# Performance work log

Measured on AMD Instinct MI355X. Metric: run time of the kernel, lower is better.

Reference implementation:

```python
import jax, jax.numpy as jnp
import numpy as np
import math

B, S, H, NH = 2, 2048, 1024, 16
DK = H // NH


def setup_inputs() -> dict:
    key = jax.random.key(0)
    ks = jax.random.split(key, 12)
    s = 1.0 / math.sqrt(H)
    return {
        "query": jax.random.normal(ks[0], (B, S, H), jnp.float32),
        "key": jax.random.normal(ks[1], (B, S, H), jnp.float32),
        "value": jax.random.normal(ks[2], (B, S, H), jnp.float32),
        "attention_mask": jax.random.randint(ks[3], (B, S), 0, 2, jnp.int32),
        "Wq": jax.random.normal(ks[4], (H, H), jnp.float32) * s,
        "bq": jnp.zeros((H,), jnp.float32),
        "Wk": jax.random.normal(ks[5], (H, H), jnp.float32) * s,
        "bk": jnp.zeros((H,), jnp.float32),
        "Wv": jax.random.normal(ks[6], (H, H), jnp.float32) * s,
        "bv": jnp.zeros((H,), jnp.float32),
        "Wo": jax.random.normal(ks[7], (H, H), jnp.float32) * s,
        "bo": jnp.zeros((H,), jnp.float32),
    }


def reference(query, key, value, attention_mask, Wq, bq, Wk, bk, Wv, bv, Wo, bo):
    # linear projections (torch Linear: x @ W^T + b)
    q = query @ Wq.T + bq
    k = key @ Wk.T + bk
    v = value @ Wv.T + bv
    # [B, S, H] -> [B, NH, S, DK]
    q = q.reshape(B, S, NH, DK).transpose(0, 2, 1, 3)
    k = k.reshape(B, S, NH, DK).transpose(0, 2, 1, 3)
    v = v.reshape(B, S, NH, DK).transpose(0, 2, 1, 3)
    # scaled dot-product scores [B, NH, S, S]
    scores = jnp.einsum("bhqd,bhkd->bhqk", q, k) / math.sqrt(DK)
    # faithful to original: masked positions set to 1e-9 (NOT -inf)
    mask = attention_mask[:, None, None, :]  # [B,1,1,S]
    scores = jnp.where(mask == 0, jnp.float32(1e-9), scores)
    weights = jax.nn.softmax(scores, axis=-1)
    # dropout_prob = 0.0 (eval) -> identity
    context = jnp.einsum("bhqk,bhkd->bhqd", weights, v)
    context = context.transpose(0, 2, 1, 3).reshape(B, S, H)
    return context @ Wo.T + bo
```

## Files before the change

kernel.cpp:

```cpp
#include <hip/hip_runtime.h>
#include <stdint.h>

#define B_ 2
#define S_ 2048
#define H_ 1024
#define NH_ 16
#define DK_ 64
#define M_ (B_*S_)

typedef __attribute__((ext_vector_type(8))) short short8;
typedef __attribute__((ext_vector_type(4))) float f32x4;
typedef __attribute__((ext_vector_type(4))) unsigned u32x4;

#define GLDS16(g, s) __builtin_amdgcn_global_load_lds( \
    (const __attribute__((address_space(1))) unsigned int*)(g), \
    (__attribute__((address_space(3))) unsigned int*)(s), 16, 0, 0)

__device__ __forceinline__ unsigned short f2bf(float x) {
  union { float f; unsigned u; } c; c.f = x;
  unsigned r = (c.u + 0x7FFF + ((c.u >> 16) & 1)) >> 16;
  return (unsigned short)r;
}

__device__ __forceinline__ f32x4 vmax4(f32x4 a, f32x4 b) {
  f32x4 r;
  r[0] = fmaxf(a[0], b[0]); r[1] = fmaxf(a[1], b[1]);
  r[2] = fmaxf(a[2], b[2]); r[3] = fmaxf(a[3], b[3]);
  return r;
}

__global__ void k_cvt3(const float4* __restrict__ a, const float4* __restrict__ b,
                       const float4* __restrict__ c,
                       ushort4* __restrict__ oa, ushort4* __restrict__ ob,
                       ushort4* __restrict__ oc) {
  int idx = blockIdx.x * 256 + threadIdx.x;
  int t = idx >> 20, i = idx & ((1 << 20) - 1);
  const float4* s = (t == 0) ? a : (t == 1) ? b : c;
  ushort4* o = (t == 0) ? oa : (t == 1) ? ob : oc;
  float4 v = s[i];
  ushort4 r; r.x = f2bf(v.x); r.y = f2bf(v.y); r.z = f2bf(v.z); r.w = f2bf(v.w);
  o[i] = r;
}

__global__ void k_cvtw(const float4* __restrict__ a, const float4* __restrict__ b,
                       const float4* __restrict__ c, const float4* __restrict__ d,
                       ushort4* __restrict__ oa, ushort4* __restrict__ ob,
                       ushort4* __restrict__ oc, ushort4* __restrict__ od) {
  int idx = blockIdx.x * 256 + threadIdx.x;
  int t = idx >> 18, i = idx & ((1 << 18) - 1);
  const float4* s = (t == 0) ? a : (t == 1) ? b : (t == 2) ? c : d;
  ushort4* o = (t == 0) ? oa : (t == 1) ? ob : (t == 2) ? oc : od;
  float4 v = s[i];
  ushort4 r; r.x = f2bf(v.x); r.y = f2bf(v.y); r.z = f2bf(v.z); r.w = f2bf(v.w);
  o[i] = r;
}

enum { MODE_Q = 0, MODE_K = 1, MODE_VT = 2, MODE_F32 = 3 };

__device__ __forceinline__ void gemm_body(
    const unsigned short* __restrict__ A, const unsigned short* __restrict__ Bw,
    const float* __restrict__ bias, const int* __restrict__ amask,
    void* __restrict__ Cout, int mode, int bx, int by) {
  __shared__ unsigned short As[128 * 64];
  __shared__ unsigned short Bs[128 * 64];
  const int tid = threadIdx.x;
  const int w = tid >> 6, lane = tid & 63;
  const int lr = lane & 15, hi = lane >> 4;
  const int wr = w >> 1, wc = w & 1;
  const int m0 = by * 128, n0 = bx * 128;

  f32x4 acc[4][4];
#pragma unroll
  for (int i = 0; i < 4; i++)
#pragma unroll
    for (int j = 0; j < 4; j++) acc[i][j] = (f32x4){0.f, 0.f, 0.f, 0.f};

  for (int k0 = 0; k0 < H_; k0 += 64) {
    __syncthreads();
#pragma unroll
    for (int it = 0; it < 4; ++it) {
      int c = it * 256 + tid;
      int row = c >> 3, ch = c & 7;
      const unsigned short* ga = A + (size_t)(m0 + row) * H_ + k0 + ((ch ^ (row & 7)) << 3);
      GLDS16(ga, As + (it * 256 + w * 64) * 8);
      const unsigned short* gb = Bw + (size_t)(n0 + row) * H_ + k0 + ((ch ^ (row & 7)) << 3);
      GLDS16(gb, Bs + (it * 256 + w * 64) * 8);
    }
    __syncthreads();
#pragma unroll
    for (int ks = 0; ks < 2; ++ks) {
      short8 af[4], bfg[4];
#pragma unroll
      for (int mi = 0; mi < 4; ++mi) {
        int row = wr * 64 + mi * 16 + lr;
        int ch = ((ks << 2) | hi) ^ (lr & 7);
        af[mi] = *(const short8*)((const char*)As + row * 128 + (ch << 4));
      }
#pragma unroll
      for (int ni = 0; ni < 4; ++ni) {
        int row = wc * 64 + ni * 16 + lr;
        int ch = ((ks << 2) | hi) ^ (lr & 7);
        bfg[ni] = *(const short8*)((const char*)Bs + row * 128 + (ch << 4));
      }
#pragma unroll
      for (int mi = 0; mi < 4; ++mi)
#pragma unroll
        for (int ni = 0; ni < 4; ++ni)
          acc[mi][ni] = __builtin_amdgcn_mfma_f32_16x16x32_bf16(af[mi], bfg[ni], acc[mi][ni], 0, 0, 0);
    }
  }

  float bvv[4];
#pragma unroll
  for (int ni = 0; ni < 4; ++ni) bvv[ni] = bias[n0 + wc * 64 + ni * 16 + lr];

  if (mode == MODE_Q || mode == MODE_K) {
    unsigned short* C = (unsigned short*)Cout;
    float km[4][4];
    if (mode == MODE_K) {
#pragma unroll
      for (int mi = 0; mi < 4; ++mi)
#pragma unroll
        for (int j = 0; j < 4; ++j) {
          int r = m0 + wr * 64 + mi * 16 + hi * 4 + j;
          km[mi][j] = amask[r] ? 1.0f : 0.0f;
        }
    }
#pragma unroll
    for (int mi = 0; mi < 4; ++mi)
#pragma unroll
      for (int ni = 0; ni < 4; ++ni) {
        int col = n0 + wc * 64 + ni * 16 + lr;
#pragma unroll
        for (int j = 0; j < 4; ++j) {
          int r = m0 + wr * 64 + mi * 16 + hi * 4 + j;
          float v = acc[mi][ni][j] + bvv[ni];
          v *= (mode == MODE_Q) ? 0.125f : km[mi][j];
          C[(size_t)r * H_ + col] = f2bf(v);
        }
      }
  } else if (mode == MODE_F32) {
    float* C = (float*)Cout;
#pragma unroll
    for (int mi = 0; mi < 4; ++mi)
#pragma unroll
      for (int ni = 0; ni < 4; ++ni) {
        int col = n0 + wc * 64 + ni * 16 + lr;
#pragma unroll
        for (int j = 0; j < 4; ++j) {
          int r = m0 + wr * 64 + mi * 16 + hi * 4 + j;
          C[(size_t)r * H_ + col] = acc[mi][ni][j] + bvv[ni];
        }
      }
  } else {
    unsigned short* Vt = (unsigned short*)Cout;
#pragma unroll
    for (int mi = 0; mi < 4; ++mi) {
      int rbase = m0 + wr * 64 + mi * 16 + hi * 4;
      int bb = rbase >> 11, s0 = rbase & (S_ - 1);
#pragma unroll
      for (int ni = 0; ni < 4; ++ni) {
        int col = n0 + wc * 64 + ni * 16 + lr;
        ushort4 pk;
        pk.x = f2bf(acc[mi][ni][0] + bvv[ni]);
        pk.y = f2bf(acc[mi][ni][1] + bvv[ni]);
        pk.z = f2bf(acc[mi][ni][2] + bvv[ni]);
        pk.w = f2bf(acc[mi][ni][3] + bvv[ni]);
        *(ushort4*)(Vt + (size_t)(bb * H_ + col) * S_ + s0) = pk;
      }
    }
  }
}

__global__ __launch_bounds__(256, 2) void k_gemm_qkv(
    const unsigned short* __restrict__ Xq, const unsigned short* __restrict__ Xk,
    const unsigned short* __restrict__ Xv,
    const unsigned short* __restrict__ Wqb, const unsigned short* __restrict__ Wkb,
    const unsigned short* __restrict__ Wvb,
    const float* __restrict__ bq, const float* __restrict__ bk,
    const float* __restrict__ bv, const int* __restrict__ amask,
    unsigned short* __restrict__ Qb, unsigned short* __restrict__ Kb,
    unsigned short* __restrict__ Vtb) {
  int z = blockIdx.z;
  const unsigned short* A = (z == 0) ? Xq : (z == 1) ? Xk : Xv;
  const unsigned short* W = (z == 0) ? Wqb : (z == 1) ? Wkb : Wvb;
  const float* bias = (z == 0) ? bq : (z == 1) ? bk : bv;
  void* C = (z == 0) ? (void*)Qb : (z == 1) ? (void*)Kb : (void*)Vtb;
  int mode = (z == 0) ? MODE_Q : (z == 1) ? MODE_K : MODE_VT;
  gemm_body(A, W, bias, amask, C, mode, blockIdx.x, blockIdx.y);
}

__global__ __launch_bounds__(256, 2) void k_gemm_o(
    const unsigned short* __restrict__ Ctx, const unsigned short* __restrict__ Wob,
    const float* __restrict__ bo, float* __restrict__ out) {
  gemm_body(Ctx, Wob, bo, nullptr, (void*)out, MODE_F32, blockIdx.x, blockIdx.y);
}

__global__ __launch_bounds__(256, 3) void k_attn(
    const unsigned short* __restrict__ Qb, const unsigned short* __restrict__ Kb,
    const unsigned short* __restrict__ Vtb, unsigned short* __restrict__ Ctx) {
  __shared__ unsigned short Klds[128 * 64];
  __shared__ unsigned short Vtl[4 * 64 * 32];

  const int tid = threadIdx.x;
  const int w = tid >> 6, lane = tid & 63;
  const int lr = lane & 15, hi = lane >> 4;
  int bid = (blockIdx.x & 7) * 128 + (blockIdx.x >> 3);
  const int qt = bid & 31;
  const int h = (bid >> 5) & 15;
  const int b = bid >> 9;
  const int q0 = qt * 64 + w * 16;

  short8 aq[2];
  {
    const unsigned short* qp = Qb + (size_t)(b * S_ + q0 + lr) * H_ + h * DK_ + hi * 8;
    aq[0] = *(const short8*)qp;
    aq[1] = *(const short8*)(qp + 32);
  }

  const int krow0 = 8 * (lr >> 2) + (lr & 3);

  const unsigned short* ksrc[4];
  const unsigned short* vsrc[4];
#pragma unroll
  for (int it = 0; it < 4; ++it) {
    int c = it * 256 + tid;
    int row = c >> 3, ch = c & 7;
    ksrc[it] = Kb + (size_t)(b * S_ + row) * H_ + h * DK_ + ((ch ^ (row & 7)) << 3);
    int m = c >> 8, d = (c >> 2) & 63, pc = c & 3;
    int kc = pc ^ ((d >> 1) & 3);
    vsrc[it] = Vtb + (size_t)(b * H_ + h * DK_ + d) * S_ + m * 32 + kc * 8;
  }

  f32x4 ctx[4];
#pragma unroll
  for (int nf = 0; nf < 4; ++nf) ctx[nf] = (f32x4){0.f, 0.f, 0.f, 0.f};
  float mrun = -30000.f, lrun = 0.f;

  for (int kv0 = 0; kv0 < S_; kv0 += 128) {
    __syncthreads();
#pragma unroll
    for (int it = 0; it < 4; ++it) {
      GLDS16(ksrc[it] + (size_t)kv0 * H_, Klds + (it * 256 + w * 64) * 8);
      GLDS16(vsrc[it] + kv0, Vtl + (it * 256 + w * 64) * 8);
    }
    __syncthreads();

    f32x4 sc[8];
#pragma unroll
    for (int m = 0; m < 4; ++m)
#pragma unroll
      for (int p = 0; p < 2; ++p) {
        int row = 32 * m + krow0 + 4 * p;
        int rb7 = (4 * p + (lr & 3));
        f32x4 acc = (f32x4){0.f, 0.f, 0.f, 0.f};
#pragma unroll
        for (int ks = 0; ks < 2; ++ks) {
          short8 kf = *(const short8*)((const char*)Klds + row * 128 +
                                       ((((ks << 2) | hi) ^ rb7) << 4));
          acc = __builtin_amdgcn_mfma_f32_16x16x32_bf16(kf, aq[ks], acc, 0, 0, 0);
        }
        sc[2 * m + p] = acc;
      }

    f32x4 t0 = vmax4(vmax4(sc[0], sc[1]), vmax4(sc[2], sc[3]));
    f32x4 t1 = vmax4(vmax4(sc[4], sc[5]), vmax4(sc[6], sc[7]));
    f32x4 tt = vmax4(t0, t1);
    float mx = fmaxf(fmaxf(tt[0], tt[1]), fmaxf(tt[2], tt[3]));
    mx = fmaxf(mx, __shfl_xor(mx, 16));
    mx = fmaxf(mx, __shfl_xor(mx, 32));
    float mnew = fmaxf(mrun, mx);
    float scale = __expf(mrun - mnew);
    f32x4 s4 = (f32x4){0.f, 0.f, 0.f, 0.f};
#pragma unroll
    for (int n = 0; n < 8; ++n) {
#pragma unroll
      for (int j = 0; j < 4; ++j) sc[n][j] = __expf(sc[n][j] - mnew);
      s4 += sc[n];
    }
    float ps = (s4[0] + s4[1]) + (s4[2] + s4[3]);
    ps += __shfl_xor(ps, 16);
    ps += __shfl_xor(ps, 32);
    lrun = lrun * scale + ps;
    mrun = mnew;
#pragma unroll
    for (int nf = 0; nf < 4; ++nf) ctx[nf] *= scale;

#pragma unroll
    for (int m = 0; m < 4; ++m) {
      unsigned w0, w1, w2, w3;
      asm("v_cvt_pk_bf16_f32 %0, %1, %2" : "=v"(w0) : "v"(sc[2*m][0]), "v"(sc[2*m][1]));
      asm("v_cvt_pk_bf16_f32 %0, %1, %2" : "=v"(w1) : "v"(sc[2*m][2]), "v"(sc[2*m][3]));
      asm("v_cvt_pk_bf16_f32 %0, %1, %2" : "=v"(w2) : "v"(sc[2*m+1][0]), "v"(sc[2*m+1][1]));
      asm("v_cvt_pk_bf16_f32 %0, %1, %2" : "=v"(w3) : "v"(sc[2*m+1][2]), "v"(sc[2*m+1][3]));
      u32x4 wp; wp.x = w0; wp.y = w1; wp.z = w2; wp.w = w3;
      short8 pb = __builtin_bit_cast(short8, wp);
#pragma unroll
      for (int nf = 0; nf < 4; ++nf) {
        int d = 16 * nf + lr;
        short8 vt = *(const short8*)((const char*)Vtl + m * 4096 + d * 64 +
                                     ((hi ^ ((d >> 1) & 3)) << 4));
        ctx[nf] = __builtin_amdgcn_mfma_f32_16x16x32_bf16(vt, pb, ctx[nf], 0, 0, 0);
      }
    }
  }

  float inv = 1.0f / lrun;
  unsigned short* cp = Ctx + (size_t)(b * S_ + q0 + lr) * H_ + h * DK_;
#pragma unroll
  for (int nf = 0; nf < 4; ++nf) {
    ushort4 o;
    o.x = f2bf(ctx[nf][0] * inv);
    o.y = f2bf(ctx[nf][1] * inv);
    o.z = f2bf(ctx[nf][2] * inv);
    o.w = f2bf(ctx[nf][3] * inv);
    *(ushort4*)(cp + nf * 16 + hi * 4) = o;
  }
}

extern "C" void kernel_launch(void* const* d_in, const int* in_sizes, int n_in,
                              void* d_out, int out_size, void* d_ws, size_t ws_size,
                              hipStream_t stream) {
  (void)in_sizes; (void)n_in; (void)out_size; (void)ws_size;
  const float* query = (const float*)d_in[0];
  const float* key   = (const float*)d_in[1];
  const float* value = (const float*)d_in[2];
  const int*   amask = (const int*)d_in[3];
  const float* Wq = (const float*)d_in[4];
  const float* bq = (const float*)d_in[5];
  const float* Wk = (const float*)d_in[6];
  const float* bk = (const float*)d_in[7];
  const float* Wv = (const float*)d_in[8];
  const float* bv = (const float*)d_in[9];
  const float* Wo = (const float*)d_in[10];
  const float* bo = (const float*)d_in[11];
  float* out = (float*)d_out;

  unsigned short* ws = (unsigned short*)d_ws;
  const size_t SZX = (size_t)M_ * H_;
  const size_t SZW = (size_t)H_ * H_;
  unsigned short* Xq  = ws;
  unsigned short* Xk  = Xq + SZX;
  unsigned short* Xv  = Xk + SZX;
  unsigned short* Wqb = Xv + SZX;
  unsigned short* Wkb = Wqb + SZW;
  unsigned short* Wvb = Wkb + SZW;
  unsigned short* Wob = Wvb + SZW;
  unsigned short* Qb  = Wob + SZW;
  unsigned short* Kb  = Qb + SZX;
  unsigned short* Vtb = Kb + SZX;
  unsigned short* Ctx = Vtb + SZX;

  k_cvt3<<<dim3(12288), dim3(256), 0, stream>>>(
      (const float4*)query, (const float4*)key, (const float4*)value,
      (ushort4*)Xq, (ushort4*)Xk, (ushort4*)Xv);
  k_cvtw<<<dim3(4096), dim3(256), 0, stream>>>(
      (const float4*)Wq, (const float4*)Wk, (const float4*)Wv, (const float4*)Wo,
      (ushort4*)Wqb, (ushort4*)Wkb, (ushort4*)Wvb, (ushort4*)Wob);
  k_gemm_qkv<<<dim3(8, 32, 3), dim3(256), 0, stream>>>(
      Xq, Xk, Xv, Wqb, Wkb, Wvb, bq, bk, bv, amask, Qb, Kb, Vtb);
  k_attn<<<dim3(1024), dim3(256), 0, stream>>>(Qb, Kb, Vtb, Ctx);
  k_gemm_o<<<dim3(8, 32), dim3(256), 0, stream>>>(Ctx, Wob, bo, out);
}
```

Measured before the change: 231.0 us.

## Rewrite attention kernel with 32x32x16 MFMA and 128-query tiles

Switches the attention kernel from 16x16x32 to 32x32x16 bf16 MFMA. Each wave now owns 32 query rows, so a block covers 128 queries and the grid halves to 512 blocks. The KV step drops to 64 keys with smaller K and V LDS tiles, and the K-row permutation and swizzle are redone to match the new fragment layout. The aim is more work per instruction and more K/V reuse per LDS load, at the cost of more registers per thread, lower occupancy (launch bounds 2), and half as many blocks to fill the GPU.

```diff
diff --git a/kernel.cpp b/kernel.cpp
--- a/kernel.cpp
+++ b/kernel.cpp
@@ -10,6 +10,7 @@
 
 typedef __attribute__((ext_vector_type(8))) short short8;
 typedef __attribute__((ext_vector_type(4))) float f32x4;
+typedef __attribute__((ext_vector_type(16))) float f32x16;
 typedef __attribute__((ext_vector_type(4))) unsigned u32x4;
 
 #define GLDS16(g, s) __builtin_amdgcn_global_load_lds( \
@@ -20,13 +21,6 @@
   union { float f; unsigned u; } c; c.f = x;
   unsigned r = (c.u + 0x7FFF + ((c.u >> 16) & 1)) >> 16;
   return (unsigned short)r;
-}
-
-__device__ __forceinline__ f32x4 vmax4(f32x4 a, f32x4 b) {
-  f32x4 r;
-  r[0] = fmaxf(a[0], b[0]); r[1] = fmaxf(a[1], b[1]);
-  r[2] = fmaxf(a[2], b[2]); r[3] = fmaxf(a[3], b[3]);
-  return r;
 }
 
 __global__ void k_cvt3(const float4* __restrict__ a, const float4* __restrict__ b,
@@ -196,126 +190,131 @@
   gemm_body(Ctx, Wob, bo, nullptr, (void*)out, MODE_F32, blockIdx.x, blockIdx.y);
 }
 
-__global__ __launch_bounds__(256, 3) void k_attn(
+__global__ __launch_bounds__(256, 2) void k_attn(
     const unsigned short* __restrict__ Qb, const unsigned short* __restrict__ Kb,
     const unsigned short* __restrict__ Vtb, unsigned short* __restrict__ Ctx) {
-  __shared__ unsigned short Klds[128 * 64];
-  __shared__ unsigned short Vtl[4 * 64 * 32];
+  __shared__ unsigned short Klds[64 * 64];
+  __shared__ unsigned short Vtl[64 * 64];
 
   const int tid = threadIdx.x;
   const int w = tid >> 6, lane = tid & 63;
-  const int lr = lane & 15, hi = lane >> 4;
-  int bid = (blockIdx.x & 7) * 128 + (blockIdx.x >> 3);
-  const int qt = bid & 31;
-  const int h = (bid >> 5) & 15;
-  const int b = bid >> 9;
-  const int q0 = qt * 64 + w * 16;
-
-  short8 aq[2];
+  const int l5 = lane & 31, hi5 = lane >> 5;
+  int bid = (blockIdx.x & 7) * 64 + (blockIdx.x >> 3);
+  const int qt = bid & 15;
+  const int h = (bid >> 4) & 15;
+  const int b = bid >> 8;
+  const int qr = qt * 128 + w * 32 + l5;
+
+  short8 aq[4];
   {
-    const unsigned short* qp = Qb + (size_t)(b * S_ + q0 + lr) * H_ + h * DK_ + hi * 8;
-    aq[0] = *(const short8*)qp;
-    aq[1] = *(const short8*)(qp + 32);
-  }
-
-  const int krow0 = 8 * (lr >> 2) + (lr & 3);
-
-  const unsigned short* ksrc[4];
-  const unsigned short* vsrc[4];
-#pragma unroll
-  for (int it = 0; it < 4; ++it) {
+    const unsigned short* qp = Qb + (size_t)(b * S_ + qr) * H_ + h * DK_ + hi5 * 8;
+#pragma unroll
+    for (int dkblk = 0; dkblk < 4; ++dkblk)
+      aq[dkblk] = *(const short8*)(qp + dkblk * 16);
+  }
+
+  const unsigned short* ksrc[2];
+  const unsigned short* vsrc[2];
+#pragma unroll
+  for (int it = 0; it < 2; ++it) {
     int c = it * 256 + tid;
-    int row = c >> 3, ch = c & 7;
-    ksrc[it] = Kb + (size_t)(b * S_ + row) * H_ + h * DK_ + ((ch ^ (row & 7)) << 3);
-    int m = c >> 8, d = (c >> 2) & 63, pc = c & 3;
-    int kc = pc ^ ((d >> 1) & 3);
-    vsrc[it] = Vtb + (size_t)(b * H_ + h * DK_ + d) * S_ + m * 32 + kc * 8;
-  }
-
-  f32x4 ctx[4];
-#pragma unroll
-  for (int nf = 0; nf < 4; ++nf) ctx[nf] = (f32x4){0.f, 0.f, 0.f, 0.f};
+    int rho = c >> 3, cl = c & 7;
+    int kap = 32 * (rho >> 5) + ((rho & 19) | ((rho & 4) << 1) | ((rho & 8) >> 1));
+    ksrc[it] = Kb + (size_t)(b * S_ + kap) * H_ + h * DK_ + ((cl ^ (rho & 7)) << 3);
+    vsrc[it] = Vtb + (size_t)(b * H_ + h * DK_ + rho) * S_ + ((cl ^ (rho & 7)) << 3);
+  }
+
+  f32x16 ctx[2];
+#pragma unroll
+  for (int dblk = 0; dblk < 2; ++dblk)
+#pragma unroll
+    for (int i = 0; i < 16; ++i) ctx[dblk][i] = 0.f;
   float mrun = -30000.f, lrun = 0.f;
 
-  for (int kv0 = 0; kv0 < S_; kv0 += 128) {
+  for (int kv0 = 0; kv0 < S_; kv0 += 64) {
     __syncthreads();
 #pragma unroll
-    for (int it = 0; it < 4; ++it) {
+    for (int it = 0; it < 2; ++it) {
       GLDS16(ksrc[it] + (size_t)kv0 * H_, Klds + (it * 256 + w * 64) * 8);
       GLDS16(vsrc[it] + kv0, Vtl + (it * 256 + w * 64) * 8);
     }
     __syncthreads();
 
-    f32x4 sc[8];
-#pragma unroll
-    for (int m = 0; m < 4; ++m)
-#pragma unroll
-      for (int p = 0; p < 2; ++p) {
-        int row = 32 * m + krow0 + 4 * p;
-        int rb7 = (4 * p + (lr & 3));
-        f32x4 acc = (f32x4){0.f, 0.f, 0.f, 0.f};
-#pragma unroll
-        for (int ks = 0; ks < 2; ++ks) {
-          short8 kf = *(const short8*)((const char*)Klds + row * 128 +
-                                       ((((ks << 2) | hi) ^ rb7) << 4));
-          acc = __builtin_amdgcn_mfma_f32_16x16x32_bf16(kf, aq[ks], acc, 0, 0, 0);
-        }
-        sc[2 * m + p] = acc;
-      }
-
-    f32x4 t0 = vmax4(vmax4(sc[0], sc[1]), vmax4(sc[2], sc[3]));
-    f32x4 t1 = vmax4(vmax4(sc[4], sc[5]), vmax4(sc[6], sc[7]));
-    f32x4 tt = vmax4(t0, t1);
-    float mx = fmaxf(fmaxf(tt[0], tt[1]), fmaxf(tt[2], tt[3]));
-    mx = fmaxf(mx, __shfl_xor(mx, 16));
+    f32x16 sc[2];
+#pragma unroll
+    for (int kb = 0; kb < 2; ++kb) {
+      f32x16 a;
+#pragma unroll
+      for (int i = 0; i < 16; ++i) a[i] = 0.f;
+#pragma unroll
+      for (int dkblk = 0; dkblk < 4; ++dkblk) {
+        int row = kb * 32 + l5;
+        int ch = (2 * dkblk + hi5) ^ (row & 7);
+        short8 kf = *(const short8*)((const char*)Klds + row * 128 + (ch << 4));
+        a = __builtin_amdgcn_mfma_f32_32x32x16_bf16(kf, aq[dkblk], a, 0, 0, 0);
+      }
+      sc[kb] = a;
+    }
+
+    float mx = sc[0][0];
+#pragma unroll
+    for (int i = 1; i < 16; ++i) mx = fmaxf(mx, sc[0][i]);
+#pragma unroll
+    for (int i = 0; i < 16; ++i) mx = fmaxf(mx, sc[1][i]);
     mx = fmaxf(mx, __shfl_xor(mx, 32));
     float mnew = fmaxf(mrun, mx);
     float scale = __expf(mrun - mnew);
-    f32x4 s4 = (f32x4){0.f, 0.f, 0.f, 0.f};
-#pragma unroll
-    for (int n = 0; n < 8; ++n) {
-#pragma unroll
-      for (int j = 0; j < 4; ++j) sc[n][j] = __expf(sc[n][j] - mnew);
-      s4 += sc[n];
-    }
-    float ps = (s4[0] + s4[1]) + (s4[2] + s4[3]);
-    ps += __shfl_xor(ps, 16);
+    float ps = 0.f;
+#pragma unroll
+    for (int kb = 0; kb < 2; ++kb)
+#pragma unroll
+      for (int i = 0; i < 16; ++i) {
+        float e = __expf(sc[kb][i] - mnew);
+        sc[kb][i] = e;
+        ps += e;
+      }
     ps += __shfl_xor(ps, 32);
     lrun = lrun * scale + ps;
     mrun = mnew;
 #pragma unroll
-    for (int nf = 0; nf < 4; ++nf) ctx[nf] *= scale;
-
-#pragma unroll
-    for (int m = 0; m < 4; ++m) {
-      unsigned w0, w1, w2, w3;
-      asm("v_cvt_pk_bf16_f32 %0, %1, %2" : "=v"(w0) : "v"(sc[2*m][0]), "v"(sc[2*m][1]));
-      asm("v_cvt_pk_bf16_f32 %0, %1, %2" : "=v"(w1) : "v"(sc[2*m][2]), "v"(sc[2*m][3]));
-      asm("v_cvt_pk_bf16_f32 %0, %1, %2" : "=v"(w2) : "v"(sc[2*m+1][0]), "v"(sc[2*m+1][1]));
-      asm("v_cvt_pk_bf16_f32 %0, %1, %2" : "=v"(w3) : "v"(sc[2*m+1][2]), "v"(sc[2*m+1][3]));
-      u32x4 wp; wp.x = w0; wp.y = w1; wp.z = w2; wp.w = w3;
-      short8 pb = __builtin_bit_cast(short8, wp);
-#pragma unroll
-      for (int nf = 0; nf < 4; ++nf) {
-        int d = 16 * nf + lr;
-        short8 vt = *(const short8*)((const char*)Vtl + m * 4096 + d * 64 +
-                                     ((hi ^ ((d >> 1) & 3)) << 4));
-        ctx[nf] = __builtin_amdgcn_mfma_f32_16x16x32_bf16(vt, pb, ctx[nf], 0, 0, 0);
-      }
-    }
+    for (int dblk = 0; dblk < 2; ++dblk)
+#pragma unroll
+      for (int i = 0; i < 16; ++i) ctx[dblk][i] *= scale;
+
+#pragma unroll
+    for (int kb = 0; kb < 2; ++kb)
+#pragma unroll
+      for (int u = 0; u < 2; ++u) {
+        unsigned w0, w1, w2, w3;
+        asm("v_cvt_pk_bf16_f32 %0, %1, %2" : "=v"(w0) : "v"(sc[kb][8*u+0]), "v"(sc[kb][8*u+1]));
+        asm("v_cvt_pk_bf16_f32 %0, %1, %2" : "=v"(w1) : "v"(sc[kb][8*u+2]), "v"(sc[kb][8*u+3]));
+        asm("v_cvt_pk_bf16_f32 %0, %1, %2" : "=v"(w2) : "v"(sc[kb][8*u+4]), "v"(sc[kb][8*u+5]));
+        asm("v_cvt_pk_bf16_f32 %0, %1, %2" : "=v"(w3) : "v"(sc[kb][8*u+6]), "v"(sc[kb][8*u+7]));
+        u32x4 wp; wp.x = w0; wp.y = w1; wp.z = w2; wp.w = w3;
+        short8 pb = __builtin_bit_cast(short8, wp);
+#pragma unroll
+        for (int dblk = 0; dblk < 2; ++dblk) {
+          int row = dblk * 32 + l5;
+          int ch = (4 * kb + 2 * u + hi5) ^ (row & 7);
+          short8 vt = *(const short8*)((const char*)Vtl + row * 128 + (ch << 4));
+          ctx[dblk] = __builtin_amdgcn_mfma_f32_32x32x16_bf16(vt, pb, ctx[dblk], 0, 0, 0);
+        }
+      }
   }
 
   float inv = 1.0f / lrun;
-  unsigned short* cp = Ctx + (size_t)(b * S_ + q0 + lr) * H_ + h * DK_;
-#pragma unroll
-  for (int nf = 0; nf < 4; ++nf) {
-    ushort4 o;
-    o.x = f2bf(ctx[nf][0] * inv);
-    o.y = f2bf(ctx[nf][1] * inv);
-    o.z = f2bf(ctx[nf][2] * inv);
-    o.w = f2bf(ctx[nf][3] * inv);
-    *(ushort4*)(cp + nf * 16 + hi * 4) = o;
-  }
+  unsigned short* cp = Ctx + (size_t)(b * S_ + qr) * H_ + h * DK_;
+#pragma unroll
+  for (int dblk = 0; dblk < 2; ++dblk)
+#pragma unroll
+    for (int s = 0; s < 4; ++s) {
+      ushort4 o;
+      o.x = f2bf(ctx[dblk][4*s+0] * inv);
+      o.y = f2bf(ctx[dblk][4*s+1] * inv);
+      o.z = f2bf(ctx[dblk][4*s+2] * inv);
+      o.w = f2bf(ctx[dblk][4*s+3] * inv);
+      *(ushort4*)(cp + dblk * 32 + 8 * s + 4 * hi5) = o;
+    }
 }
 
 extern "C" void kernel_launch(void* const* d_in, const int* in_sizes, int n_in,
@@ -359,6 +358,6 @@
       (ushort4*)Wqb, (ushort4*)Wkb, (ushort4*)Wvb, (ushort4*)Wob);
   k_gemm_qkv<<<dim3(8, 32, 3), dim3(256), 0, stream>>>(
       Xq, Xk, Xv, Wqb, Wkb, Wvb, bq, bk, bv, amask, Qb, Kb, Vtb);
-  k_attn<<<dim3(1024), dim3(256), 0, stream>>>(Qb, Kb, Vtb, Ctx);
+  k_attn<<<dim3(512), dim3(256), 0, stream>>>(Qb, Kb, Vtb, Ctx);
   k_gemm_o<<<dim3(8, 32), dim3(256), 0, stream>>>(Ctx, Wob, bo, out);
 }
```

Result: no change. 227.6 us (-1.5%).
